# Kernel tuning notes

Hardware: AMD Instinct MI355X
Metric: run time of the kernel (lower is better)

Reference implementation:

```python
import jax, jax.numpy as jnp
import numpy as np

C_IN, C_OUT, K, DG, PAD = 256, 256, 3, 2, 1
EPS = 1e-5


def setup_inputs() -> dict:
    key = jax.random.key(0)
    k = jax.random.split(key, 8)
    B, H, W = 4, 64, 64
    x = jax.random.normal(k[0], (B, C_IN, H, W), jnp.float32)
    # offset/mask conv (DCNv2 pack): 3 * dg * k * k output channels
    w_off = jax.random.normal(k[1], (3 * DG * K * K, C_IN, K, K), jnp.float32) * 0.01
    b_off = jnp.zeros((3 * DG * K * K,), jnp.float32)
    # main deformable conv weight
    w = jax.random.normal(k[2], (C_OUT, C_IN, K, K), jnp.float32) * (1.0 / np.sqrt(C_IN * K * K))
    b = jnp.zeros((C_OUT,), jnp.float32)
    # BatchNorm (eval mode: running stats)
    gamma = jnp.ones((C_OUT,), jnp.float32)
    beta = jnp.zeros((C_OUT,), jnp.float32)
    running_mean = jax.random.normal(k[3], (C_OUT,), jnp.float32) * 0.1
    running_var = jax.random.uniform(k[4], (C_OUT,), jnp.float32, 0.5, 1.5)
    return dict(x=x, w_off=w_off, b_off=b_off, w=w, b=b, gamma=gamma, beta=beta,
                running_mean=running_mean, running_var=running_var)


def _conv2d_same(x, w, b):
    y = jax.lax.conv_general_dilated(x, w, (1, 1), 'SAME',
                                     dimension_numbers=('NCHW', 'OIHW', 'NCHW'))
    return y + b[None, :, None, None]


def _deform_conv(x, w_off, b_off, w, b):
    B, C, H, W = x.shape
    K2 = K * K
    Cg = C // DG
    # offsets + modulation mask from internal conv (DCNv2 pack)
    om = _conv2d_same(x, w_off, b_off)            # [B, 3*DG*K2, H, W]
    o1, o2, m = jnp.split(om, 3, axis=1)
    mask = jax.nn.sigmoid(m).reshape(B, DG, 1, K2, H * W)
    off_y = o1.reshape(B, DG, K2, H, W)
    off_x = o2.reshape(B, DG, K2, H, W)
    # base sampling grid: output pixel + kernel tap - pad
    ki = jnp.arange(K)
    ky = (jnp.repeat(ki, K) - PAD).astype(jnp.float32)   # [K2]
    kx = (jnp.tile(ki, K) - PAD).astype(jnp.float32)     # [K2]
    py = off_y + ky[:, None, None] + jnp.arange(H, dtype=jnp.float32)[None, :, None]
    px = off_x + kx[:, None, None] + jnp.arange(W, dtype=jnp.float32)[None, None, :]
    y0 = jnp.floor(py)
    x0 = jnp.floor(px)
    ly = (py - y0).reshape(B, DG, 1, K2, H * W)
    lx = (px - x0).reshape(B, DG, 1, K2, H * W)
    y0i = y0.astype(jnp.int32)
    x0i = x0.astype(jnp.int32)
    xg = x.reshape(B, DG, Cg, H * W)

    def gather(yi, xi):
        # zero-padded bilinear corner gather, per deformable group
        valid = (yi >= 0) & (yi < H) & (xi >= 0) & (xi < W)
        lin = jnp.clip(yi, 0, H - 1) * W + jnp.clip(xi, 0, W - 1)
        v = jnp.take_along_axis(xg[:, :, :, None, :],
                                lin.reshape(B, DG, 1, K2, H * W), axis=-1)
        return v * valid.reshape(B, DG, 1, K2, H * W)

    val = (gather(y0i, x0i) * (1 - ly) * (1 - lx)
           + gather(y0i, x0i + 1) * (1 - ly) * lx
           + gather(y0i + 1, x0i) * ly * (1 - lx)
           + gather(y0i + 1, x0i + 1) * ly * lx)
    val = val * mask                               # [B, DG, Cg, K2, H*W]
    wr = w.reshape(C_OUT, DG, Cg, K2)
    out = jnp.einsum('bgckn,ogck->bon', val, wr).reshape(B, C_OUT, H, W)
    return out + b[None, :, None, None]


def reference(x, w_off, b_off, w, b, gamma, beta, running_mean, running_var):
    y = _deform_conv(x, w_off, b_off, w, b)
    inv = gamma / jnp.sqrt(running_var + EPS)
    y = (y - running_mean[None, :, None, None]) * inv[None, :, None, None] + beta[None, :, None, None]
    return jax.nn.relu(y)
```

## Files before the change

### kernel.cpp

```cpp
#include <hip/hip_runtime.h>
#include <math.h>

typedef __bf16 bf16x8 __attribute__((ext_vector_type(8)));
typedef float  f32x4  __attribute__((ext_vector_type(4)));
typedef int    i32x4  __attribute__((ext_vector_type(4)));

#define MFMA16(a, b, c) __builtin_amdgcn_mfma_f32_16x16x32_bf16((a), (b), (c), 0, 0, 0)

#define ATIDX(r, c) ((r) * 128 + (((c) ^ ((r) & 7)) * 8))

__global__ __launch_bounds__(256) void setup_kernel(
    const float* __restrict__ x, const float* __restrict__ w,
    const float* __restrict__ w_off, const float* __restrict__ bconv,
    const float* __restrict__ gamma, const float* __restrict__ beta,
    const float* __restrict__ mean, const float* __restrict__ var,
    __bf16* __restrict__ xT, __bf16* __restrict__ wFragD,
    __bf16* __restrict__ wFragO, float* __restrict__ sc,
    float* __restrict__ sh) {
  int t = threadIdx.x;
  if (blockIdx.x < 1024) {
    __shared__ float xs[64][65];
    int b = blockIdx.x >> 8, y = (blockIdx.x >> 2) & 63, cc = blockIdx.x & 3;
    const float* xb = x + (((size_t)b * 256 + cc * 64) * 64 + y) * 64;
    #pragma unroll
    for (int r = 0; r < 4; ++r) {
      int cl = r * 16 + (t >> 4), xc = (t & 15) * 4;
      f32x4 v = *(const f32x4*)(xb + (size_t)cl * 4096 + xc);
      xs[cl][xc] = v.x; xs[cl][xc + 1] = v.y;
      xs[cl][xc + 2] = v.z; xs[cl][xc + 3] = v.w;
    }
    __syncthreads();
    __bf16* dst = xT + (((size_t)b * 64 + y) * 64) * 256 + cc * 64;
    #pragma unroll
    for (int it = 0; it < 2; ++it) {
      int w2 = t + it * 256;
      int xc = w2 >> 3, cl8 = (w2 & 7) * 8;
      bf16x8 o;
      #pragma unroll
      for (int e = 0; e < 8; ++e) o[e] = (__bf16)xs[cl8 + e][xc];
      *(bf16x8*)(dst + (size_t)xc * 256 + cl8) = o;
    }
    return;
  }
  if (blockIdx.x < 1312) {
    int u = (blockIdx.x - 1024) * 256 + t;
    int lane = u & 63, ocb = (u >> 6) & 15, kc = (u >> 10) & 3, gk = u >> 12;
    int oc = ocb * 16 + (lane & 15);
    int cb = kc * 32 + (lane >> 4) * 8;
    int g = gk / 9, ktap = gk % 9;
    const float* src = w + ((size_t)oc * 256 + g * 128 + cb) * 9 + ktap;
    bf16x8 o;
    #pragma unroll
    for (int j = 0; j < 8; ++j) o[j] = (__bf16)src[(size_t)j * 9];
    *(bf16x8*)(wFragD + (size_t)u * 8) = o;
    return;
  }
  if (blockIdx.x < 1384) {
    int u = (blockIdx.x - 1312) * 256 + t;
    int lane = u & 63, ocq = (u >> 6) & 3, kc = (u >> 8) & 7, tap = u >> 11;
    int oc = ocq * 16 + (lane & 15);
    int cb = kc * 32 + (lane >> 4) * 8;
    bf16x8 o;
    #pragma unroll
    for (int j = 0; j < 8; ++j) o[j] = (__bf16)0.f;
    if (oc < 54) {
      const float* src = w_off + ((size_t)oc * 256 + cb) * 9 + tap;
      #pragma unroll
      for (int j = 0; j < 8; ++j) o[j] = (__bf16)src[(size_t)j * 9];
    }
    *(bf16x8*)(wFragO + (size_t)u * 8) = o;
    return;
  }
  if (t < 256) {
    float s = gamma[t] * rsqrtf(var[t] + 1e-5f);
    sc[t] = s;
    sh[t] = (bconv[t] - mean[t]) * s + beta[t];
  }
}

struct PhaseC {
  f32x4 swgtv[18 * 64];
  i32x4 slinv[18 * 64];
  __bf16 atile[2][2][64 * 128];
};
union FusedLDS {
  __bf16 rowbuf[3 * 66 * 256];
  PhaseC c;
};

__global__ __launch_bounds__(1024) void fused_kernel(
    const __bf16* __restrict__ xT, const __bf16* __restrict__ wFragD,
    const __bf16* __restrict__ wFragO, const float* __restrict__ b_off,
    const float* __restrict__ sc, const float* __restrict__ sh,
    float* __restrict__ out) {
  __shared__ __attribute__((aligned(16))) FusedLDS U;
  __shared__ float omrow[2][54 * 64];
  int t = threadIdx.x;
  int b = blockIdx.x >> 6, y = blockIdx.x & 63;
  int lane = t & 63, wv = t >> 6;
  int l15 = lane & 15, quad = lane >> 4;
  const __bf16* xTb = xT + (size_t)b * 64 * 64 * 256;
  bf16x8 z8;
  #pragma unroll
  for (int e = 0; e < 8; ++e) z8[e] = (__bf16)0.f;

  for (int i = t; i < 3 * 66 * 32; i += 1024) {
    int c = i & 31, px66 = (i >> 5) % 66, dy = i / 2112;
    int y2 = y + dy - 1, x2 = px66 - 1;
    bf16x8 v = z8;
    if (y2 >= 0 && y2 < 64 && x2 >= 0 && x2 < 64)
      v = *(const bf16x8*)(xTb + ((size_t)y2 * 64 + x2) * 256 + c * 8);
    *(bf16x8*)&U.rowbuf[dy * 16896 + px66 * 256 + ((c ^ (px66 & 7)) * 8)] = v;
  }
  __syncthreads();

  {
    int kh = wv & 1, ocq = (wv >> 1) & 3, mh = wv >> 3;
    f32x4 acc0 = {0.f, 0.f, 0.f, 0.f};
    f32x4 acc1 = {0.f, 0.f, 0.f, 0.f};
    for (int tap = 0; tap < 9; ++tap) {
      int dy = tap / 3, dxs = tap % 3;
      const __bf16* bb =
          wFragO + ((size_t)(tap * 8 + kh * 4) * 4 + ocq) * 512 + lane * 8;
      bf16x8 Bf[4];
      #pragma unroll
      for (int kcl = 0; kcl < 4; ++kcl)
        Bf[kcl] = *(const bf16x8*)(bb + (size_t)kcl * 4 * 512);
      int p0 = mh * 32 + l15 + dxs, p1 = p0 + 16;
      const __bf16* rb = U.rowbuf + dy * 16896;
      #pragma unroll
      for (int kcl = 0; kcl < 4; ++kcl) {
        int c = (kh * 4 + kcl) * 4 + quad;
        bf16x8 a0 = *(const bf16x8*)&rb[p0 * 256 + ((c ^ (p0 & 7)) * 8)];
        bf16x8 a1 = *(const bf16x8*)&rb[p1 * 256 + ((c ^ (p1 & 7)) * 8)];
        acc0 = MFMA16(a0, Bf[kcl], acc0);
        acc1 = MFMA16(a1, Bf[kcl], acc1);
      }
    }
    int oc = ocq * 16 + l15;
    if (oc < 54) {
      #pragma unroll
      for (int fm = 0; fm < 2; ++fm) {
        f32x4 v = fm ? acc1 : acc0;
        int pxs = mh * 32 + fm * 16 + quad * 4;
        *(f32x4*)&omrow[kh][oc * 64 + pxs] = v;
      }
    }
  }
  __syncthreads();

  for (int i = t; i < 18 * 64; i += 1024) {
    int gk = i >> 6, p = i & 63;
    int k = gk % 9;
    float oy = omrow[0][gk * 64 + p] + omrow[1][gk * 64 + p] + b_off[gk];
    float ox = omrow[0][(18 + gk) * 64 + p] + omrow[1][(18 + gk) * 64 + p]
             + b_off[18 + gk];
    float mz = omrow[0][(36 + gk) * 64 + p] + omrow[1][(36 + gk) * 64 + p]
             + b_off[36 + gk];
    float mv = 1.f / (1.f + expf(-mz));
    float py  = (float)(y + (k / 3) - 1) + oy;
    float pxf = (float)(p + (k % 3) - 1) + ox;
    float y0f = floorf(py), x0f = floorf(pxf);
    int y0 = (int)y0f, x0 = (int)x0f;
    float ly = py - y0f, lx = pxf - x0f;
    int y1 = y0 + 1, x1 = x0 + 1;
    bool vy0 = (y0 >= 0) && (y0 < 64), vy1 = (y1 >= 0) && (y1 < 64);
    bool vx0 = (x0 >= 0) && (x0 < 64), vx1 = (x1 >= 0) && (x1 < 64);
    int cy0 = min(max(y0, 0), 63), cy1 = min(max(y1, 0), 63);
    int cx0 = min(max(x0, 0), 63), cx1 = min(max(x1, 0), 63);
    f32x4 sv;
    sv.x = (vy0 && vx0) ? (1.f - ly) * (1.f - lx) * mv : 0.f;
    sv.y = (vy0 && vx1) ? (1.f - ly) * lx * mv : 0.f;
    sv.z = (vy1 && vx0) ? ly * (1.f - lx) * mv : 0.f;
    sv.w = (vy1 && vx1) ? ly * lx * mv : 0.f;
    i32x4 lv;
    lv.x = (cy0 * 64 + cx0) * 256;
    lv.y = (cy0 * 64 + cx1) * 256;
    lv.z = (cy1 * 64 + cx0) * 256;
    lv.w = (cy1 * 64 + cx1) * 256;
    U.c.swgtv[i] = sv;
    U.c.slinv[i] = lv;
  }

  f32x4 acc[4];
  #pragma unroll
  for (int fm = 0; fm < 4; ++fm) acc[fm] = (f32x4){0.f, 0.f, 0.f, 0.f};

  __syncthreads();

  int ch0 = l15 * 8;
  int p = wv * 4 + quad;
  #pragma unroll
  for (int t2 = 0; t2 < 2; ++t2) {
    const __bf16* xg = xTb + ch0;
    f32x4 sv = U.c.swgtv[t2 * 64 + p];
    i32x4 lv = U.c.slinv[t2 * 64 + p];
    bf16x8 c0 = *(const bf16x8*)(xg + lv.x);
    bf16x8 c1 = *(const bf16x8*)(xg + lv.y);
    bf16x8 c2 = *(const bf16x8*)(xg + lv.z);
    bf16x8 c3 = *(const bf16x8*)(xg + lv.w);
    bf16x8 o;
    #pragma unroll
    for (int e = 0; e < 8; ++e)
      o[e] = (__bf16)(sv.x * (float)c0[e] + sv.y * (float)c1[e]
                    + sv.z * (float)c2[e] + sv.w * (float)c3[e]);
    *(bf16x8*)&U.c.atile[0][t2][ATIDX(p, l15)] = o;
  }

  for (int iv = 0; iv < 9; ++iv) {
    __syncthreads();
    bf16x8 Bf0[4], Bf1[4];
    {
      const __bf16* bb0 =
          wFragD + ((size_t)(2 * iv) * 4 * 16 + wv) * 512 + lane * 8;
      const __bf16* bb1 = bb0 + (size_t)4 * 16 * 512;
      #pragma unroll
      for (int kc = 0; kc < 4; ++kc)
        Bf0[kc] = *(const bf16x8*)(bb0 + (size_t)kc * 16 * 512);
      #pragma unroll
      for (int kc = 0; kc < 4; ++kc)
        Bf1[kc] = *(const bf16x8*)(bb1 + (size_t)kc * 16 * 512);
    }
    bf16x8 cr[2][4];
    f32x4 sv[2];
    if (iv < 8) {
      #pragma unroll
      for (int t2 = 0; t2 < 2; ++t2) {
        int gn = 2 * iv + 2 + t2;
        const __bf16* xg = xTb + (gn / 9) * 128 + ch0;
        sv[t2] = U.c.swgtv[gn * 64 + p];
        i32x4 lv = U.c.slinv[gn * 64 + p];
        cr[t2][0] = *(const bf16x8*)(xg + lv.x);
        cr[t2][1] = *(const bf16x8*)(xg + lv.y);
        cr[t2][2] = *(const bf16x8*)(xg + lv.z);
        cr[t2][3] = *(const bf16x8*)(xg + lv.w);
      }
    }
    __builtin_amdgcn_sched_barrier(0);
    {
      const __bf16* at0 = U.c.atile[iv & 1][0];
      #pragma unroll
      for (int kc = 0; kc < 4; ++kc) {
        #pragma unroll
        for (int fm = 0; fm < 4; ++fm) {
          bf16x8 a = *(const bf16x8*)&at0[ATIDX(fm * 16 + l15, kc * 4 + quad)];
          acc[fm] = MFMA16(a, Bf0[kc], acc[fm]);
        }
      }
      const __bf16* at1 = U.c.atile[iv & 1][1];
      #pragma unroll
      for (int kc = 0; kc < 4; ++kc) {
        #pragma unroll
        for (int fm = 0; fm < 4; ++fm) {
          bf16x8 a = *(const bf16x8*)&at1[ATIDX(fm * 16 + l15, kc * 4 + quad)];
          acc[fm] = MFMA16(a, Bf1[kc], acc[fm]);
        }
      }
    }
    __builtin_amdgcn_sched_barrier(0);
    if (iv < 8) {
      #pragma unroll
      for (int t2 = 0; t2 < 2; ++t2) {
        __bf16* dst = U.c.atile[(iv + 1) & 1][t2];
        bf16x8 o;
        #pragma unroll
        for (int e = 0; e < 8; ++e)
          o[e] = (__bf16)(sv[t2].x * (float)cr[t2][0][e]
                        + sv[t2].y * (float)cr[t2][1][e]
                        + sv[t2].z * (float)cr[t2][2][e]
                        + sv[t2].w * (float)cr[t2][3][e]);
        *(bf16x8*)&dst[ATIDX(p, l15)] = o;
      }
    }
  }

  {
    int oc = wv * 16 + l15;
    float s = sc[oc], h = sh[oc];
    #pragma unroll
    for (int fm = 0; fm < 4; ++fm) {
      f32x4 v = acc[fm];
      f32x4 r = {fmaxf(v.x * s + h, 0.f), fmaxf(v.y * s + h, 0.f),
                 fmaxf(v.z * s + h, 0.f), fmaxf(v.w * s + h, 0.f)};
      int pxs = fm * 16 + quad * 4;
      *(f32x4*)(out + (((size_t)b * 256 + oc) * 64 + y) * 64 + pxs) = r;
    }
  }
}

extern "C" void kernel_launch(void* const* d_in, const int* in_sizes, int n_in,
                              void* d_out, int out_size, void* d_ws, size_t ws_size,
                              hipStream_t stream) {
  const float* x     = (const float*)d_in[0];
  const float* w_off = (const float*)d_in[1];
  const float* b_off = (const float*)d_in[2];
  const float* w     = (const float*)d_in[3];
  const float* bconv = (const float*)d_in[4];
  const float* gamma = (const float*)d_in[5];
  const float* beta  = (const float*)d_in[6];
  const float* rmean = (const float*)d_in[7];
  const float* rvar  = (const float*)d_in[8];
  float* out = (float*)d_out;

  __bf16* xT     = (__bf16*)d_ws;
  __bf16* wFragD = (__bf16*)((char*)d_ws + 8388608);
  __bf16* wFragO = (__bf16*)((char*)d_ws + 9568256);
  float*  sc     = (float*)((char*)d_ws + 9863168);
  float*  sh     = (float*)((char*)d_ws + 9864192);

  setup_kernel<<<1385, 256, 0, stream>>>(
      x, w, w_off, bconv, gamma, beta, rmean, rvar, xT, wFragD, wFragO, sc, sh);
  fused_kernel<<<4 * 64, 1024, 0, stream>>>(xT, wFragD, wFragO, b_off, sc, sh, out);
}
```

Measured before the change: 129.5 us.

## Retile MFMA work to 2x2 fragments per wave and pipeline single-tap A tiles

The main deformable GEMM now gives each wave a 2x2 block of 16x16 output fragments (two pixel rows by two oc blocks) instead of 1x4, so each A fragment read from LDS feeds two MFMAs. The A tile now holds one tap at a time with double buffering, using one barrier per tap. The gather for tap t+2 is issued before the MFMAs of tap t so the gather latency overlaps compute. The offset conv is similarly retiled so each A read is shared across two oc blocks. The cost is more barriers, twice the B-fragment registers per wave and a smaller LDS footprint per stage.

```diff
diff --git a/kernel.cpp b/kernel.cpp
--- a/kernel.cpp
+++ b/kernel.cpp
@@ -81,7 +81,7 @@
 struct PhaseC {
   f32x4 swgtv[18 * 64];
   i32x4 slinv[18 * 64];
-  __bf16 atile[2][2][64 * 128];
+  __bf16 atile[2][64 * 128];
 };
 union FusedLDS {
   __bf16 rowbuf[3 * 66 * 256];
@@ -115,51 +115,50 @@
   __syncthreads();
 
   {
-    int kh = wv & 1, ocq = (wv >> 1) & 3, mh = wv >> 3;
+    int kh = wv & 1, pxt = (wv >> 1) & 3, ocd = wv >> 3;
     f32x4 acc0 = {0.f, 0.f, 0.f, 0.f};
     f32x4 acc1 = {0.f, 0.f, 0.f, 0.f};
     for (int tap = 0; tap < 9; ++tap) {
       int dy = tap / 3, dxs = tap % 3;
       const __bf16* bb =
-          wFragO + ((size_t)(tap * 8 + kh * 4) * 4 + ocq) * 512 + lane * 8;
-      bf16x8 Bf[4];
-      #pragma unroll
-      for (int kcl = 0; kcl < 4; ++kcl)
-        Bf[kcl] = *(const bf16x8*)(bb + (size_t)kcl * 4 * 512);
-      int p0 = mh * 32 + l15 + dxs, p1 = p0 + 16;
+          wFragO + ((size_t)(tap * 8 + kh * 4) * 4 + ocd * 2) * 512 + lane * 8;
+      bf16x8 Bf0[4], Bf1[4];
+      #pragma unroll
+      for (int kcl = 0; kcl < 4; ++kcl) {
+        Bf0[kcl] = *(const bf16x8*)(bb + (size_t)kcl * 4 * 512);
+        Bf1[kcl] = *(const bf16x8*)(bb + (size_t)kcl * 4 * 512 + 512);
+      }
+      int p0 = pxt * 16 + l15 + dxs;
       const __bf16* rb = U.rowbuf + dy * 16896;
       #pragma unroll
       for (int kcl = 0; kcl < 4; ++kcl) {
         int c = (kh * 4 + kcl) * 4 + quad;
         bf16x8 a0 = *(const bf16x8*)&rb[p0 * 256 + ((c ^ (p0 & 7)) * 8)];
-        bf16x8 a1 = *(const bf16x8*)&rb[p1 * 256 + ((c ^ (p1 & 7)) * 8)];
-        acc0 = MFMA16(a0, Bf[kcl], acc0);
-        acc1 = MFMA16(a1, Bf[kcl], acc1);
-      }
-    }
-    int oc = ocq * 16 + l15;
-    if (oc < 54) {
-      #pragma unroll
-      for (int fm = 0; fm < 2; ++fm) {
-        f32x4 v = fm ? acc1 : acc0;
-        int pxs = mh * 32 + fm * 16 + quad * 4;
-        *(f32x4*)&omrow[kh][oc * 64 + pxs] = v;
-      }
+        acc0 = MFMA16(a0, Bf0[kcl], acc0);
+        acc1 = MFMA16(a0, Bf1[kcl], acc1);
+      }
+    }
+    #pragma unroll
+    for (int fo = 0; fo < 2; ++fo) {
+      f32x4 v = fo ? acc1 : acc0;
+      int oc = (ocd * 2 + fo) * 16 + l15;
+      if (oc < 54)
+        *(f32x4*)&omrow[kh][oc * 64 + pxt * 16 + quad * 4] = v;
     }
   }
   __syncthreads();
 
   for (int i = t; i < 18 * 64; i += 1024) {
-    int gk = i >> 6, p = i & 63;
+    int gk = i >> 6, pb = i & 63;
     int k = gk % 9;
-    float oy = omrow[0][gk * 64 + p] + omrow[1][gk * 64 + p] + b_off[gk];
-    float ox = omrow[0][(18 + gk) * 64 + p] + omrow[1][(18 + gk) * 64 + p]
+    float oy = omrow[0][gk * 64 + pb] + omrow[1][gk * 64 + pb] + b_off[gk];
+    float ox = omrow[0][(18 + gk) * 64 + pb] + omrow[1][(18 + gk) * 64 + pb]
              + b_off[18 + gk];
-    float mz = omrow[0][(36 + gk) * 64 + p] + omrow[1][(36 + gk) * 64 + p]
+    float mz = omrow[0][(36 + gk) * 64 + pb] + omrow[1][(36 + gk) * 64 + pb]
              + b_off[36 + gk];
     float mv = 1.f / (1.f + expf(-mz));
     float py  = (float)(y + (k / 3) - 1) + oy;
-    float pxf = (float)(p + (k % 3) - 1) + ox;
+    float pxf = (float)(pb + (k % 3) - 1) + ox;
     float y0f = floorf(py), x0f = floorf(pxf);
     int y0 = (int)y0f, x0 = (int)x0f;
     float ly = py - y0f, lx = pxf - x0f;
@@ -182,19 +181,25 @@
     U.c.slinv[i] = lv;
   }
 
-  f32x4 acc[4];
+  int ocp = wv & 7, fmh = wv >> 3;
+  f32x4 acc[2][2];
   #pragma unroll
-  for (int fm = 0; fm < 4; ++fm) acc[fm] = (f32x4){0.f, 0.f, 0.f, 0.f};
+  for (int fm = 0; fm < 2; ++fm)
+    #pragma unroll
+    for (int fn = 0; fn < 2; ++fn)
+      acc[fm][fn] = (f32x4){0.f, 0.f, 0.f, 0.f};
 
   __syncthreads();
 
   int ch0 = l15 * 8;
   int p = wv * 4 + quad;
-  #pragma unroll
-  for (int t2 = 0; t2 < 2; ++t2) {
+
+  bf16x8 crA[4], crB[4];
+  f32x4 svA, svB;
+  {
+    f32x4 sv = U.c.swgtv[p];
+    i32x4 lv = U.c.slinv[p];
     const __bf16* xg = xTb + ch0;
-    f32x4 sv = U.c.swgtv[t2 * 64 + p];
-    i32x4 lv = U.c.slinv[t2 * 64 + p];
     bf16x8 c0 = *(const bf16x8*)(xg + lv.x);
     bf16x8 c1 = *(const bf16x8*)(xg + lv.y);
     bf16x8 c2 = *(const bf16x8*)(xg + lv.z);
@@ -204,85 +209,118 @@
     for (int e = 0; e < 8; ++e)
       o[e] = (__bf16)(sv.x * (float)c0[e] + sv.y * (float)c1[e]
                     + sv.z * (float)c2[e] + sv.w * (float)c3[e]);
-    *(bf16x8*)&U.c.atile[0][t2][ATIDX(p, l15)] = o;
-  }
-
-  for (int iv = 0; iv < 9; ++iv) {
+    *(bf16x8*)&U.c.atile[0][ATIDX(p, l15)] = o;
+  }
+  {
+    svB = U.c.swgtv[64 + p];
+    i32x4 lv = U.c.slinv[64 + p];
+    const __bf16* xg = xTb + ch0;
+    crB[0] = *(const bf16x8*)(xg + lv.x);
+    crB[1] = *(const bf16x8*)(xg + lv.y);
+    crB[2] = *(const bf16x8*)(xg + lv.z);
+    crB[3] = *(const bf16x8*)(xg + lv.w);
+  }
+
+  for (int ivp = 0; ivp < 9; ++ivp) {
+    int t0 = 2 * ivp;
     __syncthreads();
-    bf16x8 Bf0[4], Bf1[4];
-    {
-      const __bf16* bb0 =
-          wFragD + ((size_t)(2 * iv) * 4 * 16 + wv) * 512 + lane * 8;
-      const __bf16* bb1 = bb0 + (size_t)4 * 16 * 512;
-      #pragma unroll
-      for (int kc = 0; kc < 4; ++kc)
-        Bf0[kc] = *(const bf16x8*)(bb0 + (size_t)kc * 16 * 512);
-      #pragma unroll
-      for (int kc = 0; kc < 4; ++kc)
-        Bf1[kc] = *(const bf16x8*)(bb1 + (size_t)kc * 16 * 512);
-    }
-    bf16x8 cr[2][4];
-    f32x4 sv[2];
-    if (iv < 8) {
-      #pragma unroll
-      for (int t2 = 0; t2 < 2; ++t2) {
-        int gn = 2 * iv + 2 + t2;
-        const __bf16* xg = xTb + (gn / 9) * 128 + ch0;
-        sv[t2] = U.c.swgtv[gn * 64 + p];
-        i32x4 lv = U.c.slinv[gn * 64 + p];
-        cr[t2][0] = *(const bf16x8*)(xg + lv.x);
-        cr[t2][1] = *(const bf16x8*)(xg + lv.y);
-        cr[t2][2] = *(const bf16x8*)(xg + lv.z);
-        cr[t2][3] = *(const bf16x8*)(xg + lv.w);
-      }
+    bf16x8 Bf[8];
+    {
+      const __bf16* bb =
+          wFragD + ((size_t)(t0 * 4) * 16 + ocp * 2) * 512 + lane * 8;
+      #pragma unroll
+      for (int kc = 0; kc < 4; ++kc) {
+        Bf[kc * 2]     = *(const bf16x8*)(bb + (size_t)kc * 16 * 512);
+        Bf[kc * 2 + 1] = *(const bf16x8*)(bb + (size_t)kc * 16 * 512 + 512);
+      }
+    }
+    if (ivp < 8) {
+      int gn = t0 + 2;
+      const __bf16* xg = xTb + (gn / 9) * 128 + ch0;
+      svA = U.c.swgtv[gn * 64 + p];
+      i32x4 lv = U.c.slinv[gn * 64 + p];
+      crA[0] = *(const bf16x8*)(xg + lv.x);
+      crA[1] = *(const bf16x8*)(xg + lv.y);
+      crA[2] = *(const bf16x8*)(xg + lv.z);
+      crA[3] = *(const bf16x8*)(xg + lv.w);
     }
     __builtin_amdgcn_sched_barrier(0);
     {
-      const __bf16* at0 = U.c.atile[iv & 1][0];
       #pragma unroll
       for (int kc = 0; kc < 4; ++kc) {
         #pragma unroll
-        for (int fm = 0; fm < 4; ++fm) {
-          bf16x8 a = *(const bf16x8*)&at0[ATIDX(fm * 16 + l15, kc * 4 + quad)];
-          acc[fm] = MFMA16(a, Bf0[kc], acc[fm]);
+        for (int fm = 0; fm < 2; ++fm) {
+          bf16x8 a = *(const bf16x8*)
+              &U.c.atile[0][ATIDX((fmh * 2 + fm) * 16 + l15, kc * 4 + quad)];
+          acc[fm][0] = MFMA16(a, Bf[kc * 2],     acc[fm][0]);
+          acc[fm][1] = MFMA16(a, Bf[kc * 2 + 1], acc[fm][1]);
         }
       }
-      const __bf16* at1 = U.c.atile[iv & 1][1];
+    }
+    __builtin_amdgcn_sched_barrier(0);
+    {
+      bf16x8 o;
+      #pragma unroll
+      for (int e = 0; e < 8; ++e)
+        o[e] = (__bf16)(svB.x * (float)crB[0][e] + svB.y * (float)crB[1][e]
+                      + svB.z * (float)crB[2][e] + svB.w * (float)crB[3][e]);
+      *(bf16x8*)&U.c.atile[1][ATIDX(p, l15)] = o;
+    }
+    __syncthreads();
+    int t1 = t0 + 1;
+    {
+      const __bf16* bb =
+          wFragD + ((size_t)(t1 * 4) * 16 + ocp * 2) * 512 + lane * 8;
+      #pragma unroll
+      for (int kc = 0; kc < 4; ++kc) {
+        Bf[kc * 2]     = *(const bf16x8*)(bb + (size_t)kc * 16 * 512);
+        Bf[kc * 2 + 1] = *(const bf16x8*)(bb + (size_t)kc * 16 * 512 + 512);
+      }
+    }
+    if (ivp < 8) {
+      int gn = t1 + 2;
+      const __bf16* xg = xTb + (gn / 9) * 128 + ch0;
+      svB = U.c.swgtv[gn * 64 + p];
+      i32x4 lv = U.c.slinv[gn * 64 + p];
+      crB[0] = *(const bf16x8*)(xg + lv.x);
+      crB[1] = *(const bf16x8*)(xg + lv.y);
+      crB[2] = *(const bf16x8*)(xg + lv.z);
+      crB[3] = *(const bf16x8*)(xg + lv.w);
+    }
+    __builtin_amdgcn_sched_barrier(0);
+    {
       #pragma unroll
       for (int kc = 0; kc < 4; ++kc) {
         #pragma unroll
-        for (int fm = 0; fm < 4; ++fm) {
-          bf16x8 a = *(const bf16x8*)&at1[ATIDX(fm * 16 + l15, kc * 4 + quad)];
-          acc[fm] = MFMA16(a, Bf1[kc], acc[fm]);
+        for (int fm = 0; fm < 2; ++fm) {
+          bf16x8 a = *(const bf16x8*)
+              &U.c.atile[1][ATIDX((fmh * 2 + fm) * 16 + l15, kc * 4 + quad)];
+          acc[fm][0] = MFMA16(a, Bf[kc * 2],     acc[fm][0]);
+          acc[fm][1] = MFMA16(a, Bf[kc * 2 + 1], acc[fm][1]);
         }
       }
     }
     __builtin_amdgcn_sched_barrier(0);
-    if (iv < 8) {
-      #pragma unroll
-      for (int t2 = 0; t2 < 2; ++t2) {
-        __bf16* dst = U.c.atile[(iv + 1) & 1][t2];
-        bf16x8 o;
-        #pragma unroll
-        for (int e = 0; e < 8; ++e)
-          o[e] = (__bf16)(sv[t2].x * (float)cr[t2][0][e]
-                        + sv[t2].y * (float)cr[t2][1][e]
-                        + sv[t2].z * (float)cr[t2][2][e]
-                        + sv[t2].w * (float)cr[t2][3][e]);
-        *(bf16x8*)&dst[ATIDX(p, l15)] = o;
-      }
-    }
-  }
-
-  {
-    int oc = wv * 16 + l15;
-    float s = sc[oc], h = sh[oc];
-    #pragma unroll
-    for (int fm = 0; fm < 4; ++fm) {
-      f32x4 v = acc[fm];
+    if (ivp < 8) {
+      bf16x8 o;
+      #pragma unroll
+      for (int e = 0; e < 8; ++e)
+        o[e] = (__bf16)(svA.x * (float)crA[0][e] + svA.y * (float)crA[1][e]
+                      + svA.z * (float)crA[2][e] + svA.w * (float)crA[3][e]);
+      *(bf16x8*)&U.c.atile[0][ATIDX(p, l15)] = o;
+    }
+  }
+
+  #pragma unroll
+  for (int fm = 0; fm < 2; ++fm) {
+    #pragma unroll
+    for (int fn = 0; fn < 2; ++fn) {
+      int oc = (ocp * 2 + fn) * 16 + l15;
+      float s = sc[oc], h = sh[oc];
+      f32x4 v = acc[fm][fn];
       f32x4 r = {fmaxf(v.x * s + h, 0.f), fmaxf(v.y * s + h, 0.f),
                  fmaxf(v.z * s + h, 0.f), fmaxf(v.w * s + h, 0.f)};
-      int pxs = fm * 16 + quad * 4;
+      int pxs = (fmh * 2 + fm) * 16 + quad * 4;
       *(f32x4*)(out + (((size_t)b * 256 + oc) * 64 + y) * 64 + pxs) = r;
     }
   }
```

Measured after the change: 135.5 us. +4.6%, slower.

## Remap block-to-row order and re-tile offset conv MFMA across pixels

Applied to the files above, without the earlier changes.

Blocks are now assigned so that consecutive block IDs interleave batches and adjacent rows. The likely aim is to spread work across the chiplets' L2 caches and improve reuse of shared rows. In the offset/mask conv, each wave now computes one 16-pixel tile against two output-channel tiles, reusing each A fragment from LDS. Previously it computed two pixel tiles against one channel tile. This halves the LDS A reads but doubles the per-wave B (weight) global loads. The waves with ocd=1 partly compute channel tiles 48-63 that are discarded.

```diff
diff --git a/kernel.cpp b/kernel.cpp
--- a/kernel.cpp
+++ b/kernel.cpp
@@ -96,7 +96,9 @@
   __shared__ __attribute__((aligned(16))) FusedLDS U;
   __shared__ float omrow[2][54 * 64];
   int t = threadIdx.x;
-  int b = blockIdx.x >> 6, y = blockIdx.x & 63;
+  int bid = blockIdx.x;
+  int b = (bid & 7) >> 1;
+  int y = ((bid >> 3) << 1) | (bid & 1);
   int lane = t & 63, wv = t >> 6;
   int l15 = lane & 15, quad = lane >> 4;
   const __bf16* xTb = xT + (size_t)b * 64 * 64 * 256;
@@ -115,51 +117,50 @@
   __syncthreads();
 
   {
-    int kh = wv & 1, ocq = (wv >> 1) & 3, mh = wv >> 3;
+    int kh = wv & 1, pxt = (wv >> 1) & 3, ocd = wv >> 3;
     f32x4 acc0 = {0.f, 0.f, 0.f, 0.f};
     f32x4 acc1 = {0.f, 0.f, 0.f, 0.f};
     for (int tap = 0; tap < 9; ++tap) {
       int dy = tap / 3, dxs = tap % 3;
       const __bf16* bb =
-          wFragO + ((size_t)(tap * 8 + kh * 4) * 4 + ocq) * 512 + lane * 8;
-      bf16x8 Bf[4];
-      #pragma unroll
-      for (int kcl = 0; kcl < 4; ++kcl)
-        Bf[kcl] = *(const bf16x8*)(bb + (size_t)kcl * 4 * 512);
-      int p0 = mh * 32 + l15 + dxs, p1 = p0 + 16;
+          wFragO + ((size_t)(tap * 8 + kh * 4) * 4 + ocd * 2) * 512 + lane * 8;
+      bf16x8 Bf0[4], Bf1[4];
+      #pragma unroll
+      for (int kcl = 0; kcl < 4; ++kcl) {
+        Bf0[kcl] = *(const bf16x8*)(bb + (size_t)kcl * 4 * 512);
+        Bf1[kcl] = *(const bf16x8*)(bb + (size_t)kcl * 4 * 512 + 512);
+      }
+      int p0 = pxt * 16 + l15 + dxs;
       const __bf16* rb = U.rowbuf + dy * 16896;
       #pragma unroll
       for (int kcl = 0; kcl < 4; ++kcl) {
         int c = (kh * 4 + kcl) * 4 + quad;
         bf16x8 a0 = *(const bf16x8*)&rb[p0 * 256 + ((c ^ (p0 & 7)) * 8)];
-        bf16x8 a1 = *(const bf16x8*)&rb[p1 * 256 + ((c ^ (p1 & 7)) * 8)];
-        acc0 = MFMA16(a0, Bf[kcl], acc0);
-        acc1 = MFMA16(a1, Bf[kcl], acc1);
-      }
-    }
-    int oc = ocq * 16 + l15;
-    if (oc < 54) {
-      #pragma unroll
-      for (int fm = 0; fm < 2; ++fm) {
-        f32x4 v = fm ? acc1 : acc0;
-        int pxs = mh * 32 + fm * 16 + quad * 4;
-        *(f32x4*)&omrow[kh][oc * 64 + pxs] = v;
-      }
+        acc0 = MFMA16(a0, Bf0[kcl], acc0);
+        acc1 = MFMA16(a0, Bf1[kcl], acc1);
+      }
+    }
+    #pragma unroll
+    for (int fo = 0; fo < 2; ++fo) {
+      f32x4 v = fo ? acc1 : acc0;
+      int oc = (ocd * 2 + fo) * 16 + l15;
+      if (oc < 54)
+        *(f32x4*)&omrow[kh][oc * 64 + pxt * 16 + quad * 4] = v;
     }
   }
   __syncthreads();
 
   for (int i = t; i < 18 * 64; i += 1024) {
-    int gk = i >> 6, p = i & 63;
+    int gk = i >> 6, pb = i & 63;
     int k = gk % 9;
-    float oy = omrow[0][gk * 64 + p] + omrow[1][gk * 64 + p] + b_off[gk];
-    float ox = omrow[0][(18 + gk) * 64 + p] + omrow[1][(18 + gk) * 64 + p]
+    float oy = omrow[0][gk * 64 + pb] + omrow[1][gk * 64 + pb] + b_off[gk];
+    float ox = omrow[0][(18 + gk) * 64 + pb] + omrow[1][(18 + gk) * 64 + pb]
              + b_off[18 + gk];
-    float mz = omrow[0][(36 + gk) * 64 + p] + omrow[1][(36 + gk) * 64 + p]
+    float mz = omrow[0][(36 + gk) * 64 + pb] + omrow[1][(36 + gk) * 64 + pb]
              + b_off[36 + gk];
     float mv = 1.f / (1.f + expf(-mz));
     float py  = (float)(y + (k / 3) - 1) + oy;
-    float pxf = (float)(p + (k % 3) - 1) + ox;
+    float pxf = (float)(pb + (k % 3) - 1) + ox;
     float y0f = floorf(py), x0f = floorf(pxf);
     int y0 = (int)y0f, x0 = (int)x0f;
     float ly = py - y0f, lx = pxf - x0f;
```

Measured after the change: 130.7 us. About the same (+1.0%).
